# Kernel optimization log

Hardware: AMD Instinct MI355X
Metric: run time of the kernel (lower is better)

The kernel has to match this reference:

```python
import jax, jax.numpy as jnp
import numpy as np
from jax import lax

C = 128
HEADS = 8
WS = 8
HIDDEN = C * 4


def _ln2d(x, w, b, eps=1e-6):
    # channel-first LayerNorm over dim 1 of [B,C,H,W]
    u = x.mean(axis=1, keepdims=True)
    s = ((x - u) ** 2).mean(axis=1, keepdims=True)
    xh = (x - u) / jnp.sqrt(s + eps)
    return w[None, :, None, None] * xh + b[None, :, None, None]


def _partition(x, ws):
    # [B,C,H,W] -> [B*nW, ws*ws, C]
    B, C_, H, W = x.shape
    x = x.transpose(0, 2, 3, 1)  # BHWC
    x = x.reshape(B, H // ws, ws, W // ws, ws, C_)
    x = x.transpose(0, 1, 3, 2, 4, 5)
    return x.reshape(-1, ws * ws, C_)


def _reverse(x, ws, H, W, B):
    # [B*nW, ws*ws, C] -> [B,C,H,W]
    C_ = x.shape[-1]
    x = x.reshape(B, H // ws, W // ws, ws, ws, C_)
    x = x.transpose(0, 1, 3, 2, 4, 5).reshape(B, H, W, C_)
    return x.transpose(0, 3, 1, 2)


def setup_inputs() -> dict:
    key = jax.random.key(0)
    ks = jax.random.split(key, 16)
    B, H, W = 4, 256, 256
    inp = {
        "x": jax.random.normal(ks[0], (B, C, H, W), jnp.float32),
        "l0": jax.random.uniform(ks[1], (B, 1, H, W), jnp.float32),
        "norm1_w": jnp.ones((C,), jnp.float32),
        "norm1_b": jnp.zeros((C,), jnp.float32),
        "norm2_w": jnp.ones((C,), jnp.float32),
        "norm2_b": jnp.zeros((C,), jnp.float32),
        "qkv_w": jax.random.normal(ks[2], (3 * C, C), jnp.float32) * (1.0 / np.sqrt(C)),
        "gate_w": jax.random.normal(ks[3], (C,), jnp.float32),
        "gate_b": jnp.zeros((C,), jnp.float32),
        "proj_w": jax.random.normal(ks[4], (C, C), jnp.float32) * (1.0 / np.sqrt(C)),
        "proj_b": jnp.zeros((C,), jnp.float32),
        "ffn_w1": jax.random.normal(ks[5], (HIDDEN, C), jnp.float32) * (1.0 / np.sqrt(C)),
        "ffn_b1": jnp.zeros((HIDDEN,), jnp.float32),
        "ffn_dw": jax.random.normal(ks[6], (HIDDEN, 1, 3, 3), jnp.float32) * (1.0 / 3.0),
        "ffn_dwb": jnp.zeros((HIDDEN,), jnp.float32),
        "ffn_w2": jax.random.normal(ks[7], (C, HIDDEN), jnp.float32) * (1.0 / np.sqrt(HIDDEN)),
        "ffn_b2": jnp.zeros((C,), jnp.float32),
    }
    return inp


def reference(x, l0, norm1_w, norm1_b, norm2_w, norm2_b, qkv_w, gate_w, gate_b,
              proj_w, proj_b, ffn_w1, ffn_b1, ffn_dw, ffn_dwb, ffn_w2, ffn_b2):
    B, C_, H, W = x.shape
    ws = WS
    # H,W chosen divisible by ws -> no padding branch
    head_dim = C_ // HEADS
    scale = head_dim ** -0.5

    shortcut = x
    xn = _ln2d(x, norm1_w, norm1_b)
    qkv = jnp.einsum("oc,bchw->bohw", qkv_w, xn)
    q, k, v = jnp.split(qkv, 3, axis=1)

    # illumination gate (l0 already at [H,W]; bilinear resize to same size is identity)
    gate = jax.nn.sigmoid(l0 * gate_w[None, :, None, None] + gate_b[None, :, None, None])
    q = q * gate

    q = _partition(q, ws)  # [Bw, ws*ws, C]
    k = _partition(k, ws)
    v = _partition(v, ws)
    Bw, N, _ = q.shape
    q = q.reshape(Bw, N, HEADS, head_dim)
    k = k.reshape(Bw, N, HEADS, head_dim)
    v = v.reshape(Bw, N, HEADS, head_dim)

    attn = jnp.einsum("bqhd,bkhd->bhqk", q, k) * scale
    attn = jax.nn.softmax(attn, axis=-1)
    out = jnp.einsum("bhqk,bkhd->bqhd", attn, v).reshape(Bw, N, C_)
    out = _reverse(out, ws, H, W, B)

    out = jnp.einsum("oc,bchw->bohw", proj_w, out) + proj_b[None, :, None, None]
    out = out + shortcut

    # FFN: 1x1 -> GELU -> depthwise 3x3 -> GELU -> 1x1
    h = _ln2d(out, norm2_w, norm2_b)
    h = jnp.einsum("oc,bchw->bohw", ffn_w1, h) + ffn_b1[None, :, None, None]
    h = jax.nn.gelu(h, approximate=False)
    h = lax.conv_general_dilated(h, ffn_dw, window_strides=(1, 1), padding="SAME",
                                 dimension_numbers=("NCHW", "OIHW", "NCHW"),
                                 feature_group_count=HIDDEN)
    h = h + ffn_dwb[None, :, None, None]
    h = jax.nn.gelu(h, approximate=False)
    h = jnp.einsum("oc,bchw->bohw", ffn_w2, h) + ffn_b2[None, :, None, None]
    return out + h
```

## Files before the change

### kernel.cpp

```cpp
#include <hip/hip_runtime.h>
#include <hip/hip_bf16.h>

#define HW   65536
#define CHW  (128*65536)
#define QKV_OZ  33554432u
#define QKV_H   1048576u
#define QKV_WIN 1024u

typedef __attribute__((ext_vector_type(8))) short bf16x8;
typedef __attribute__((ext_vector_type(4))) float f32x4;

__device__ __forceinline__ float geluf(float v){
    float u = 0.7978845608028654f * v * (1.f + 0.044715f*v*v);
    float e = __expf(2.f*u);
    float th = 1.f - 2.f/(e+1.f);
    return 0.5f*v*(1.f+th);
}

__device__ __forceinline__ float sigmoidf_(float z){
    return 1.f / (1.f + __expf(-z));
}

__device__ __forceinline__ float bf2f(short s){
    return __uint_as_float(((unsigned)(unsigned short)s) << 16);
}

__global__ __launch_bounds__(256) void k_cvt(
    const float* __restrict__ src, __hip_bfloat16* __restrict__ dst, int n)
{
    int i = blockIdx.x*256 + threadIdx.x;
    if (i < n) dst[i] = __float2bfloat16(src[i]);
}

__global__ __launch_bounds__(256,2) void k_ln_qkv_mfma(
    const float* __restrict__ x, const float* __restrict__ l0,
    const float* __restrict__ n1w, const float* __restrict__ n1b,
    const __hip_bfloat16* __restrict__ qkvw, const float* __restrict__ gate_w,
    const float* __restrict__ gate_b, __hip_bfloat16* __restrict__ qkvb)
{
    __shared__ short sxb[128*130];
    __shared__ float sp1[256], sp2[256];
    const int t = threadIdx.x;
    const int lane = t & 63, w = t >> 6;
    const int l15 = lane & 15, q4 = (lane >> 4)*4, ko = (lane >> 4)*8;
    const int mhalf = w & 1, phalf = w >> 1;
    const int pbase = blockIdx.x * 128;
    const int b = pbase >> 16;
    const int hw0 = pbase & 65535;
    const int x0 = hw0 & 255;
    const int y  = hw0 >> 8;
    const int wy = y >> 3, ty = y & 7;
    const int pxs = t & 127, chalf = t >> 7;
    const float* xb = x + (size_t)b*CHW + (size_t)chalf*64*HW + hw0 + pxs;
    unsigned* srow = (unsigned*)sxb + pxs*65 + chalf*32;

    float s1 = 0.f, s2 = 0.f;
    #pragma unroll 8
    for (int j = 0; j < 32; ++j) {
        float v0 = xb[(size_t)(2*j)*HW];
        float v1 = xb[(size_t)(2*j+1)*HW];
        s1 += v0 + v1; s2 += v0*v0 + v1*v1;
        __hip_bfloat162 pk = __float22bfloat162_rn(make_float2(v0, v1));
        srow[j] = *(unsigned*)&pk;
    }
    sp1[pxs*2 + chalf] = s1;
    sp2[pxs*2 + chalf] = s2;
    __syncthreads();
    const float s1t = sp1[pxs*2] + sp1[pxs*2 + 1];
    const float s2t = sp2[pxs*2] + sp2[pxs*2 + 1];
    const float mean = s1t * 0.0078125f;
    const float rstd = rsqrtf(s2t*0.0078125f - mean*mean + 1e-6f);
    #pragma unroll 8
    for (int j = 0; j < 32; ++j) {
        unsigned u = srow[j];
        float v0 = __uint_as_float(u << 16);
        float v1 = __uint_as_float(u & 0xffff0000u);
        const int c = chalf*64 + 2*j;
        v0 = (v0 - mean)*rstd*n1w[c]   + n1b[c];
        v1 = (v1 - mean)*rstd*n1w[c+1] + n1b[c+1];
        __hip_bfloat162 pk = __float22bfloat162_rn(make_float2(v0, v1));
        srow[j] = *(unsigned*)&pk;
    }
    __syncthreads();

    float lv[4];
    #pragma unroll
    for (int nt = 0; nt < 4; ++nt)
        lv[nt] = l0[(size_t)b*HW + hw0 + phalf*64 + nt*16 + l15];

    unsigned toff[4];
    #pragma unroll
    for (int nt = 0; nt < 4; ++nt) {
        const int xg = x0 + phalf*64 + nt*16 + l15;
        toff[nt] = (unsigned)((wy*32 + (xg >> 3))*1024 + (ty*8 + (xg & 7))*16);
    }

    const short* wq = (const short*)qkvw;
    for (int oz = 0; oz < 3; ++oz) {
        f32x4 acc[4][4];
        #pragma unroll
        for (int mt = 0; mt < 4; ++mt)
            #pragma unroll
            for (int nt = 0; nt < 4; ++nt)
                acc[mt][nt] = (f32x4){0.f,0.f,0.f,0.f};
        #pragma unroll
        for (int kc = 0; kc < 4; ++kc) {
            bf16x8 bfrag[4];
            #pragma unroll
            for (int nt = 0; nt < 4; ++nt) {
                const int px = phalf*64 + nt*16 + l15;
                bfrag[nt] = *(const bf16x8*)(sxb + px*130 + kc*32 + ko);
            }
            #pragma unroll
            for (int mt = 0; mt < 4; ++mt) {
                const int m = oz*128 + mhalf*64 + mt*16 + l15;
                bf16x8 af = *(const bf16x8*)(wq + m*128 + kc*32 + ko);
                #pragma unroll
                for (int nt = 0; nt < 4; ++nt)
                    acc[mt][nt] = __builtin_amdgcn_mfma_f32_16x16x32_bf16(af, bfrag[nt], acc[mt][nt], 0, 0, 0);
            }
        }
        __hip_bfloat16* ob = qkvb + (size_t)oz*QKV_OZ + (size_t)b*8*QKV_H;
        #pragma unroll
        for (int mt = 0; mt < 4; ++mt) {
            const int h = mhalf*4 + mt;
            #pragma unroll
            for (int nt = 0; nt < 4; ++nt) {
                float v0 = acc[mt][nt][0], v1 = acc[mt][nt][1];
                float v2 = acc[mt][nt][2], v3 = acc[mt][nt][3];
                if (oz == 0) {
                    const int o = h*16 + q4;
                    v0 *= sigmoidf_(lv[nt]*gate_w[o]   + gate_b[o]);
                    v1 *= sigmoidf_(lv[nt]*gate_w[o+1] + gate_b[o+1]);
                    v2 *= sigmoidf_(lv[nt]*gate_w[o+2] + gate_b[o+2]);
                    v3 *= sigmoidf_(lv[nt]*gate_w[o+3] + gate_b[o+3]);
                }
                __hip_bfloat162 p0 = __float22bfloat162_rn(make_float2(v0, v1));
                __hip_bfloat162 p1 = __float22bfloat162_rn(make_float2(v2, v3));
                uint2 st;
                st.x = *(unsigned*)&p0;
                st.y = *(unsigned*)&p1;
                *(uint2*)(ob + (size_t)h*QKV_H + toff[nt] + q4) = st;
            }
        }
    }
}

__global__ __launch_bounds__(64) void k_attn(
    const __hip_bfloat16* __restrict__ qkv, float* __restrict__ attn_out)
{
    __shared__ float sk[64*17];
    __shared__ float sv[64*17];
    const int t = threadIdx.x;
    const int win = blockIdx.x;
    const int head = blockIdx.y;
    const int b = win >> 10;
    const int wi = win & 1023;
    const size_t wb = ((size_t)(b*8 + head))*QKV_H + (size_t)wi*QKV_WIN + t*16;
    const __hip_bfloat16* qp = qkv + wb;
    const __hip_bfloat16* kp = qp + QKV_OZ;
    const __hip_bfloat16* vp = qp + 2u*QKV_OZ;
    bf16x8 q0 = *(const bf16x8*)(qp);
    bf16x8 q1 = *(const bf16x8*)(qp + 8);
    bf16x8 k0 = *(const bf16x8*)(kp);
    bf16x8 k1 = *(const bf16x8*)(kp + 8);
    bf16x8 v0 = *(const bf16x8*)(vp);
    bf16x8 v1 = *(const bf16x8*)(vp + 8);
    float qr[16];
    #pragma unroll
    for (int j = 0; j < 8; ++j) {
        qr[j]   = bf2f(q0[j]);
        qr[8+j] = bf2f(q1[j]);
        sk[t*17 + j]     = bf2f(k0[j]);
        sk[t*17 + 8 + j] = bf2f(k1[j]);
        sv[t*17 + j]     = bf2f(v0[j]);
        sv[t*17 + 8 + j] = bf2f(v1[j]);
    }
    __syncthreads();
    float sc[64];
    float m = -1e30f;
    #pragma unroll
    for (int kt = 0; kt < 64; ++kt) {
        float dot = 0.f;
        #pragma unroll
        for (int d = 0; d < 16; ++d) dot = fmaf(qr[d], sk[kt*17+d], dot);
        dot *= 0.25f;
        sc[kt] = dot;
        m = fmaxf(m, dot);
    }
    float ssum = 0.f;
    #pragma unroll
    for (int kt = 0; kt < 64; ++kt) { float e = __expf(sc[kt]-m); sc[kt] = e; ssum += e; }
    const float rs = 1.f / ssum;
    float o[16];
    #pragma unroll
    for (int d = 0; d < 16; ++d) o[d] = 0.f;
    #pragma unroll
    for (int kt = 0; kt < 64; ++kt) {
        const float p = sc[kt];
        #pragma unroll
        for (int d = 0; d < 16; ++d) o[d] = fmaf(p, sv[kt*17+d], o[d]);
    }
    const int wy = wi >> 5, wx = wi & 31;
    const int ty = t >> 3, tx = t & 7;
    const size_t hw = (size_t)(wy*8 + ty)*256 + wx*8 + tx;
    float* ob = attn_out + (size_t)b*CHW + (size_t)head*16*HW + hw;
    #pragma unroll
    for (int d = 0; d < 16; ++d) ob[(size_t)d*HW] = o[d]*rs;
}

__global__ __launch_bounds__(256,2) void k_proj_mfma(
    const float* __restrict__ x, const __hip_bfloat16* __restrict__ projw,
    const float* __restrict__ proj_b, float* __restrict__ out)
{
    __shared__ short sxb[128*130];
    const int t = threadIdx.x;
    const int lane = t & 63, w = t >> 6;
    const int l15 = lane & 15, q4 = (lane >> 4)*4, ko = (lane >> 4)*8;
    const int mhalf = w & 1, phalf = w >> 1;
    const int pbase = blockIdx.x * 128;
    const int b = pbase >> 16;
    const int hw0 = pbase & 65535;
    const int pxs = t & 127, chalf = t >> 7;
    const float* ab = out + (size_t)b*CHW + (size_t)chalf*64*HW + hw0 + pxs;
    unsigned* srow = (unsigned*)sxb + pxs*65 + chalf*32;
    #pragma unroll 8
    for (int j = 0; j < 32; ++j) {
        float v0 = ab[(size_t)(2*j)*HW];
        float v1 = ab[(size_t)(2*j+1)*HW];
        __hip_bfloat162 pk = __float22bfloat162_rn(make_float2(v0, v1));
        srow[j] = *(unsigned*)&pk;
    }
    __syncthreads();
    f32x4 acc[4][4];
    #pragma unroll
    for (int mt = 0; mt < 4; ++mt)
        #pragma unroll
        for (int nt = 0; nt < 4; ++nt)
            acc[mt][nt] = (f32x4){0.f,0.f,0.f,0.f};
    const short* wp = (const short*)projw;
    #pragma unroll
    for (int kc = 0; kc < 4; ++kc) {
        bf16x8 bfrag[4];
        #pragma unroll
        for (int nt = 0; nt < 4; ++nt) {
            const int px = phalf*64 + nt*16 + l15;
            bfrag[nt] = *(const bf16x8*)(sxb + px*130 + kc*32 + ko);
        }
        #pragma unroll
        for (int mt = 0; mt < 4; ++mt) {
            const int m = mhalf*64 + mt*16 + l15;
            bf16x8 af = *(const bf16x8*)(wp + m*128 + kc*32 + ko);
            #pragma unroll
            for (int nt = 0; nt < 4; ++nt)
                acc[mt][nt] = __builtin_amdgcn_mfma_f32_16x16x32_bf16(af, bfrag[nt], acc[mt][nt], 0, 0, 0);
        }
    }
    const float* xb = x + (size_t)b*CHW + hw0;
    float* ob = out + (size_t)b*CHW + hw0;
    #pragma unroll
    for (int mt = 0; mt < 4; ++mt)
        #pragma unroll
        for (int nt = 0; nt < 4; ++nt) {
            const int px = phalf*64 + nt*16 + l15;
            #pragma unroll
            for (int r = 0; r < 4; ++r) {
                const int o = mhalf*64 + mt*16 + q4 + r;
                ob[(size_t)o*HW + px] = acc[mt][nt][r] + proj_b[o] + xb[(size_t)o*HW + px];
            }
        }
}

__global__ __launch_bounds__(256,2) void k_ffn1_mfma(
    const float* __restrict__ outb, const float* __restrict__ n2w, const float* __restrict__ n2b,
    const __hip_bfloat16* __restrict__ w1, const float* __restrict__ b1,
    __hip_bfloat16* __restrict__ h1s)
{
    __shared__ short sxb[128*130];
    __shared__ float sp1[256], sp2[256];
    const int t = threadIdx.x;
    const int lane = t & 63, w = t >> 6;
    const int l15 = lane & 15, q4 = (lane >> 4)*4, ko = (lane >> 4)*8;
    const int mhalf = w & 1, phalf = w >> 1;
    const int hw0 = blockIdx.x * 128;
    const int pxs = t & 127, chalf = t >> 7;
    const float* xb = outb + (size_t)chalf*64*HW + hw0 + pxs;
    unsigned* srow = (unsigned*)sxb + pxs*65 + chalf*32;
    float s1 = 0.f, s2 = 0.f;
    #pragma unroll 8
    for (int j = 0; j < 32; ++j) {
        float v0 = xb[(size_t)(2*j)*HW];
        float v1 = xb[(size_t)(2*j+1)*HW];
        s1 += v0 + v1; s2 += v0*v0 + v1*v1;
        __hip_bfloat162 pk = __float22bfloat162_rn(make_float2(v0, v1));
        srow[j] = *(unsigned*)&pk;
    }
    sp1[pxs*2 + chalf] = s1;
    sp2[pxs*2 + chalf] = s2;
    __syncthreads();
    const float s1t = sp1[pxs*2] + sp1[pxs*2 + 1];
    const float s2t = sp2[pxs*2] + sp2[pxs*2 + 1];
    const float mean = s1t * 0.0078125f;
    const float rstd = rsqrtf(s2t*0.0078125f - mean*mean + 1e-6f);
    #pragma unroll 8
    for (int j = 0; j < 32; ++j) {
        unsigned u = srow[j];
        float v0 = __uint_as_float(u << 16);
        float v1 = __uint_as_float(u & 0xffff0000u);
        const int c = chalf*64 + 2*j;
        v0 = (v0 - mean)*rstd*n2w[c]   + n2b[c];
        v1 = (v1 - mean)*rstd*n2w[c+1] + n2b[c+1];
        __hip_bfloat162 pk = __float22bfloat162_rn(make_float2(v0, v1));
        srow[j] = *(unsigned*)&pk;
    }
    __syncthreads();
    const short* w1s = (const short*)w1;
    __hip_bfloat16* hb = h1s + hw0;
    for (int mc = 0; mc < 4; ++mc) {
        f32x4 acc[4][4];
        #pragma unroll
        for (int mt = 0; mt < 4; ++mt)
            #pragma unroll
            for (int nt = 0; nt < 4; ++nt)
                acc[mt][nt] = (f32x4){0.f,0.f,0.f,0.f};
        #pragma unroll
        for (int kc = 0; kc < 4; ++kc) {
            bf16x8 bfrag[4];
            #pragma unroll
            for (int nt = 0; nt < 4; ++nt) {
                const int px = phalf*64 + nt*16 + l15;
                bfrag[nt] = *(const bf16x8*)(sxb + px*130 + kc*32 + ko);
            }
            #pragma unroll
            for (int mt = 0; mt < 4; ++mt) {
                const int m = mc*128 + mhalf*64 + mt*16 + l15;
                bf16x8 af = *(const bf16x8*)(w1s + m*128 + kc*32 + ko);
                #pragma unroll
                for (int nt = 0; nt < 4; ++nt)
                    acc[mt][nt] = __builtin_amdgcn_mfma_f32_16x16x32_bf16(af, bfrag[nt], acc[mt][nt], 0, 0, 0);
            }
        }
        #pragma unroll
        for (int mt = 0; mt < 4; ++mt)
            #pragma unroll
            for (int nt = 0; nt < 4; ++nt) {
                const int px = phalf*64 + nt*16 + l15;
                #pragma unroll
                for (int r = 0; r < 4; ++r) {
                    const int o = mc*128 + mhalf*64 + mt*16 + q4 + r;
                    const float v = geluf(acc[mt][nt][r] + b1[o]);
                    hb[(size_t)o*HW + px] = __float2bfloat16(v);
                }
            }
    }
}

__global__ __launch_bounds__(256) void k_dwconv(
    const __hip_bfloat16* __restrict__ h1b,
    unsigned* __restrict__ h2u,
    const float* __restrict__ dwf, const float* __restrict__ dwb)
{
    __shared__ short sh[2*18*260];
    const int t = threadIdx.x;
    const int rb = blockIdx.x & 15;
    const int cp = blockIdx.x >> 4;
    const int row0 = rb * 16;
    #pragma unroll
    for (int ch = 0; ch < 2; ++ch) {
        const __hip_bfloat16* src = h1b + (size_t)(cp*2 + ch)*HW;
        #pragma unroll
        for (int i = 0; i < 9; ++i) {
            const int idx = t + i*256;
            const int r = idx >> 7;
            const int u = idx & 127;
            const int y = row0 - 1 + r;
            unsigned v = 0u;
            if ((unsigned)y < 256u) v = *(const unsigned*)(src + (size_t)y*256 + u*2);
            *(unsigned*)(&sh[ch*4680 + r*260 + 2 + u*2]) = v;
        }
    }
    if (t < 72) {
        const int ch = t / 36, q = t - ch*36;
        const int r = q >> 1;
        sh[ch*4680 + r*260 + ((q & 1) ? 258 : 1)] = 0;
    }
    __syncthreads();
    float wt[2][9], bs[2];
    #pragma unroll
    for (int ch = 0; ch < 2; ++ch) {
        const float* dwc = dwf + (size_t)(cp*2 + ch)*9;
        #pragma unroll
        for (int k = 0; k < 9; ++k) wt[ch][k] = dwc[k];
        bs[ch] = dwb[cp*2 + ch];
    }
    const int xp = (t & 127) * 2;
    const int rh = t >> 7;
    #pragma unroll
    for (int r = 0; r < 8; ++r) {
        const int orow = rh*8 + r;
        const int y = row0 + orow;
        float res[2][2];
        #pragma unroll
        for (int ch = 0; ch < 2; ++ch) {
            const short* base = sh + ch*4680 + orow*260 + xp + 1;
            float a[3][4];
            #pragma unroll
            for (int dy = 0; dy < 3; ++dy)
                #pragma unroll
                for (int k = 0; k < 4; ++k)
                    a[dy][k] = __uint_as_float((unsigned)(unsigned short)base[dy*260 + k] << 16);
            #pragma unroll
            for (int xj = 0; xj < 2; ++xj) {
                float s = bs[ch];
                #pragma unroll
                for (int dy = 0; dy < 3; ++dy)
                    #pragma unroll
                    for (int dx = 0; dx < 3; ++dx)
                        s = fmaf(a[dy][xj+dx], wt[ch][dy*3+dx], s);
                res[ch][xj] = geluf(s);
            }
        }
        __hip_bfloat162 pk0 = __float22bfloat162_rn(make_float2(res[0][0], res[1][0]));
        __hip_bfloat162 pk1 = __float22bfloat162_rn(make_float2(res[0][1], res[1][1]));
        uint2 st;
        st.x = *(unsigned*)&pk0;
        st.y = *(unsigned*)&pk1;
        *(uint2*)(h2u + (size_t)cp*HW + (size_t)y*256 + xp) = st;
    }
}

__global__ __launch_bounds__(256,2) void k_ffn2g(
    const unsigned* __restrict__ h2u, const __hip_bfloat16* __restrict__ w2b,
    const float* __restrict__ b2, float* __restrict__ outb)
{
    __shared__ short sxb[128*130];
    const int t = threadIdx.x;
    const int lane = t & 63, w = t >> 6;
    const int l15 = lane & 15, q4 = (lane >> 4)*4, ko = (lane >> 4)*8;
    const int mhalf = w & 1, phalf = w >> 1;
    const int pbase = blockIdx.x * 128;
    const int pxs = t & 127;
    const int chalf = t >> 7;
    f32x4 acc[4][4];
    #pragma unroll
    for (int mt = 0; mt < 4; ++mt)
        #pragma unroll
        for (int nt = 0; nt < 4; ++nt)
            acc[mt][nt] = (f32x4){0.f,0.f,0.f,0.f};
    const short* w2s = (const short*)w2b;
    for (int k4 = 0; k4 < 4; ++k4) {
        if (k4) __syncthreads();
        const unsigned* hsrc = h2u + (size_t)(k4*64 + chalf*32)*HW + pbase + pxs;
        unsigned* sdst = (unsigned*)sxb + pxs*65 + chalf*32;
        #pragma unroll
        for (int c = 0; c < 32; ++c)
            sdst[c] = hsrc[(size_t)c*HW];
        __syncthreads();
        #pragma unroll
        for (int kc = 0; kc < 4; ++kc) {
            bf16x8 bfrag[4];
            #pragma unroll
            for (int nt = 0; nt < 4; ++nt) {
                const int px = phalf*64 + nt*16 + l15;
                bfrag[nt] = *(const bf16x8*)(sxb + px*130 + kc*32 + ko);
            }
            #pragma unroll
            for (int mt = 0; mt < 4; ++mt) {
                const int m = mhalf*64 + mt*16 + l15;
                bf16x8 af = *(const bf16x8*)(w2s + (size_t)m*512 + k4*128 + kc*32 + ko);
                #pragma unroll
                for (int nt = 0; nt < 4; ++nt)
                    acc[mt][nt] = __builtin_amdgcn_mfma_f32_16x16x32_bf16(af, bfrag[nt], acc[mt][nt], 0, 0, 0);
            }
        }
    }
    #pragma unroll
    for (int mt = 0; mt < 4; ++mt)
        #pragma unroll
        for (int nt = 0; nt < 4; ++nt) {
            const int px = pbase + phalf*64 + nt*16 + l15;
            #pragma unroll
            for (int r = 0; r < 4; ++r) {
                const int o = mhalf*64 + mt*16 + q4 + r;
                outb[(size_t)o*HW + px] = acc[mt][nt][r] + b2[o] + outb[(size_t)o*HW + px];
            }
        }
}

extern "C" void kernel_launch(void* const* d_in, const int* in_sizes, int n_in,
                              void* d_out, int out_size, void* d_ws, size_t ws_size,
                              hipStream_t stream) {
    const float* x      = (const float*)d_in[0];
    const float* l0     = (const float*)d_in[1];
    const float* n1w    = (const float*)d_in[2];
    const float* n1b    = (const float*)d_in[3];
    const float* n2w    = (const float*)d_in[4];
    const float* n2b    = (const float*)d_in[5];
    const float* qkv_w  = (const float*)d_in[6];
    const float* gate_w = (const float*)d_in[7];
    const float* gate_b = (const float*)d_in[8];
    const float* proj_w = (const float*)d_in[9];
    const float* proj_b = (const float*)d_in[10];
    const float* ffn_w1 = (const float*)d_in[11];
    const float* ffn_b1 = (const float*)d_in[12];
    const float* ffn_dw = (const float*)d_in[13];
    const float* ffn_dwb= (const float*)d_in[14];
    const float* ffn_w2 = (const float*)d_in[15];
    const float* ffn_b2 = (const float*)d_in[16];

    float* out = (float*)d_out;
    __hip_bfloat16* qkvb = (__hip_bfloat16*)d_ws;
    unsigned* h2u        = (unsigned*)d_ws;
    __hip_bfloat16* h1s  = (__hip_bfloat16*)((char*)d_ws + 201326592);
    char* wbase = (char*)d_ws + 268435456;
    __hip_bfloat16* qkvw_b = (__hip_bfloat16*)(wbase);
    __hip_bfloat16* projw_b= (__hip_bfloat16*)(wbase + 98304);
    __hip_bfloat16* w1b    = (__hip_bfloat16*)(wbase + 131072);
    __hip_bfloat16* w2b    = (__hip_bfloat16*)(wbase + 262144);

    k_cvt<<<dim3(192), dim3(256), 0, stream>>>(qkv_w, qkvw_b, 49152);
    k_cvt<<<dim3(64),  dim3(256), 0, stream>>>(proj_w, projw_b, 16384);
    k_cvt<<<dim3(256), dim3(256), 0, stream>>>(ffn_w1, w1b, 65536);
    k_cvt<<<dim3(256), dim3(256), 0, stream>>>(ffn_w2, w2b, 65536);

    k_ln_qkv_mfma<<<dim3(2048), dim3(256), 0, stream>>>(x, l0, n1w, n1b, qkvw_b, gate_w, gate_b, qkvb);
    k_attn       <<<dim3(4096, 8), dim3(64), 0, stream>>>(qkvb, out);
    k_proj_mfma  <<<dim3(2048), dim3(256), 0, stream>>>(x, projw_b, proj_b, out);
    for (int b = 0; b < 4; ++b) {
        k_ffn1_mfma<<<dim3(512),  dim3(256), 0, stream>>>(out + (size_t)b*CHW, n2w, n2b, w1b, ffn_b1, h1s);
        k_dwconv   <<<dim3(4096), dim3(256), 0, stream>>>(h1s, h2u, ffn_dw, ffn_dwb);
        k_ffn2g    <<<dim3(512),  dim3(256), 0, stream>>>(h2u, w2b, ffn_b2, out + (size_t)b*CHW);
    }
}
```

Before: 1.230 ms.

## Rewrite window attention with bf16 MFMA for QK^T and PV

Replaces the scalar per-thread attention kernel (one 64-thread block per window-head) with an MFMA-based kernel where each wavefront handles one window-head and four wavefronts share a block. QK^T and PV run as 16x16x32 bf16 MFMAs, with the unused half of K zero-padded. Probabilities are split into hi and lo bf16 parts and both are accumulated, so precision stays close to fp32. The aim is to remove the heavy scalar FMA and LDS traffic, at the cost of extra LDS transposes, block-wide syncs and a doubled PV pass.

```diff
diff --git a/kernel.cpp b/kernel.cpp
--- a/kernel.cpp
+++ b/kernel.cpp
@@ -8,6 +8,7 @@
 #define QKV_WIN 1024u
 
 typedef __attribute__((ext_vector_type(8))) short bf16x8;
+typedef __attribute__((ext_vector_type(4))) short bf16x4;
 typedef __attribute__((ext_vector_type(4))) float f32x4;
 
 __device__ __forceinline__ float geluf(float v){
@@ -146,67 +147,142 @@
     }
 }
 
-__global__ __launch_bounds__(64) void k_attn(
+__global__ __launch_bounds__(256) void k_attn(
     const __hip_bfloat16* __restrict__ qkv, float* __restrict__ attn_out)
 {
-    __shared__ float sk[64*17];
-    __shared__ float sv[64*17];
+    __shared__ short vt[4][16*72];
+    __shared__ short pt[4][64*68];
     const int t = threadIdx.x;
-    const int win = blockIdx.x;
-    const int head = blockIdx.y;
-    const int b = win >> 10;
-    const int wi = win & 1023;
-    const size_t wb = ((size_t)(b*8 + head))*QKV_H + (size_t)wi*QKV_WIN + t*16;
-    const __hip_bfloat16* qp = qkv + wb;
+    const int l = t & 63, w = t >> 6;
+    const int c = l & 15, g = l >> 4;
+    const int id = blockIdx.x*4 + w;
+    const int b = id >> 13;
+    const int head = (id >> 10) & 7;
+    const int wi = id & 1023;
+    const __hip_bfloat16* qp = qkv + ((size_t)(b*8 + head))*QKV_H + (size_t)wi*QKV_WIN;
     const __hip_bfloat16* kp = qp + QKV_OZ;
     const __hip_bfloat16* vp = qp + 2u*QKV_OZ;
-    bf16x8 q0 = *(const bf16x8*)(qp);
-    bf16x8 q1 = *(const bf16x8*)(qp + 8);
-    bf16x8 k0 = *(const bf16x8*)(kp);
-    bf16x8 k1 = *(const bf16x8*)(kp + 8);
-    bf16x8 v0 = *(const bf16x8*)(vp);
-    bf16x8 v1 = *(const bf16x8*)(vp + 8);
-    float qr[16];
-    #pragma unroll
-    for (int j = 0; j < 8; ++j) {
-        qr[j]   = bf2f(q0[j]);
-        qr[8+j] = bf2f(q1[j]);
-        sk[t*17 + j]     = bf2f(k0[j]);
-        sk[t*17 + 8 + j] = bf2f(k1[j]);
-        sv[t*17 + j]     = bf2f(v0[j]);
-        sv[t*17 + 8 + j] = bf2f(v1[j]);
-    }
-    __syncthreads();
-    float sc[64];
-    float m = -1e30f;
-    #pragma unroll
-    for (int kt = 0; kt < 64; ++kt) {
-        float dot = 0.f;
-        #pragma unroll
-        for (int d = 0; d < 16; ++d) dot = fmaf(qr[d], sk[kt*17+d], dot);
-        dot *= 0.25f;
-        sc[kt] = dot;
-        m = fmaxf(m, dot);
-    }
-    float ssum = 0.f;
-    #pragma unroll
-    for (int kt = 0; kt < 64; ++kt) { float e = __expf(sc[kt]-m); sc[kt] = e; ssum += e; }
-    const float rs = 1.f / ssum;
-    float o[16];
-    #pragma unroll
-    for (int d = 0; d < 16; ++d) o[d] = 0.f;
-    #pragma unroll
-    for (int kt = 0; kt < 64; ++kt) {
-        const float p = sc[kt];
-        #pragma unroll
-        for (int d = 0; d < 16; ++d) o[d] = fmaf(p, sv[kt*17+d], o[d]);
-    }
+
+    bf16x8 v0 = *(const bf16x8*)(vp + l*16);
+    bf16x8 v1 = *(const bf16x8*)(vp + l*16 + 8);
+    short* vtw = &vt[w][0];
+    #pragma unroll
+    for (int d = 0; d < 8; ++d) vtw[d*72 + l] = v0[d];
+    #pragma unroll
+    for (int d = 0; d < 8; ++d) vtw[(8+d)*72 + l] = v1[d];
+
+    bf16x8 kf[4], qf[4];
+    #pragma unroll
+    for (int mj = 0; mj < 4; ++mj) {
+        if (g < 2) {
+            kf[mj] = *(const bf16x8*)(kp + (mj*16 + c)*16 + g*8);
+            qf[mj] = *(const bf16x8*)(qp + (mj*16 + c)*16 + g*8);
+        } else {
+            kf[mj] = (bf16x8){0,0,0,0,0,0,0,0};
+            qf[mj] = (bf16x8){0,0,0,0,0,0,0,0};
+        }
+    }
+    f32x4 st[4][4];
+    #pragma unroll
+    for (int mj = 0; mj < 4; ++mj)
+        #pragma unroll
+        for (int ni = 0; ni < 4; ++ni)
+            st[mj][ni] = (f32x4){0.f,0.f,0.f,0.f};
+    #pragma unroll
+    for (int mj = 0; mj < 4; ++mj)
+        #pragma unroll
+        for (int ni = 0; ni < 4; ++ni)
+            st[mj][ni] = __builtin_amdgcn_mfma_f32_16x16x32_bf16(kf[mj], qf[ni], st[mj][ni], 0, 0, 0);
+
+    float rs[4];
+    bf16x4 pa[4][4], pb[4][4];
+    #pragma unroll
+    for (int ni = 0; ni < 4; ++ni) {
+        float mx = -1e30f;
+        #pragma unroll
+        for (int mj = 0; mj < 4; ++mj)
+            #pragma unroll
+            for (int r = 0; r < 4; ++r)
+                mx = fmaxf(mx, st[mj][ni][r]);
+        mx = fmaxf(mx, __shfl_xor(mx, 16));
+        mx = fmaxf(mx, __shfl_xor(mx, 32));
+        mx *= 0.25f;
+        float sum = 0.f;
+        #pragma unroll
+        for (int mj = 0; mj < 4; ++mj) {
+            float p[4], lo[4];
+            #pragma unroll
+            for (int r = 0; r < 4; ++r) {
+                p[r] = __expf(st[mj][ni][r]*0.25f - mx);
+                sum += p[r];
+            }
+            __hip_bfloat162 h0 = __float22bfloat162_rn(make_float2(p[0], p[1]));
+            __hip_bfloat162 h1 = __float22bfloat162_rn(make_float2(p[2], p[3]));
+            union { unsigned u[2]; bf16x4 v; } hi;
+            hi.u[0] = *(unsigned*)&h0; hi.u[1] = *(unsigned*)&h1;
+            pa[mj][ni] = hi.v;
+            #pragma unroll
+            for (int r = 0; r < 4; ++r) lo[r] = p[r] - bf2f(hi.v[r]);
+            __hip_bfloat162 g0 = __float22bfloat162_rn(make_float2(lo[0], lo[1]));
+            __hip_bfloat162 g1 = __float22bfloat162_rn(make_float2(lo[2], lo[3]));
+            union { unsigned u[2]; bf16x4 v; } lw;
+            lw.u[0] = *(unsigned*)&g0; lw.u[1] = *(unsigned*)&g1;
+            pb[mj][ni] = lw.v;
+        }
+        sum += __shfl_xor(sum, 16);
+        sum += __shfl_xor(sum, 32);
+        rs[ni] = 1.f / sum;
+    }
+
+    short* ptw = &pt[w][0];
+    f32x4 oc[4];
+    #pragma unroll
+    for (int ni = 0; ni < 4; ++ni) oc[ni] = (f32x4){0.f,0.f,0.f,0.f};
+    bf16x8 vf[2];
+    #pragma unroll
+    for (int kb = 0; kb < 2; ++kb)
+        vf[kb] = *(const bf16x8*)(vtw + c*72 + kb*32 + g*8);
+
+    #pragma unroll
+    for (int mj = 0; mj < 4; ++mj)
+        #pragma unroll
+        for (int ni = 0; ni < 4; ++ni)
+            *(bf16x4*)(ptw + (ni*16 + c)*68 + mj*16 + g*4) = pa[mj][ni];
+    __syncthreads();
+    #pragma unroll
+    for (int kb = 0; kb < 2; ++kb)
+        #pragma unroll
+        for (int ni = 0; ni < 4; ++ni) {
+            bf16x8 pf = *(const bf16x8*)(ptw + (ni*16 + c)*68 + kb*32 + g*8);
+            oc[ni] = __builtin_amdgcn_mfma_f32_16x16x32_bf16(vf[kb], pf, oc[ni], 0, 0, 0);
+        }
+    __syncthreads();
+    #pragma unroll
+    for (int mj = 0; mj < 4; ++mj)
+        #pragma unroll
+        for (int ni = 0; ni < 4; ++ni)
+            *(bf16x4*)(ptw + (ni*16 + c)*68 + mj*16 + g*4) = pb[mj][ni];
+    __syncthreads();
+    #pragma unroll
+    for (int kb = 0; kb < 2; ++kb)
+        #pragma unroll
+        for (int ni = 0; ni < 4; ++ni) {
+            bf16x8 pf = *(const bf16x8*)(ptw + (ni*16 + c)*68 + kb*32 + g*8);
+            oc[ni] = __builtin_amdgcn_mfma_f32_16x16x32_bf16(vf[kb], pf, oc[ni], 0, 0, 0);
+        }
+
     const int wy = wi >> 5, wx = wi & 31;
-    const int ty = t >> 3, tx = t & 7;
-    const size_t hw = (size_t)(wy*8 + ty)*256 + wx*8 + tx;
-    float* ob = attn_out + (size_t)b*CHW + (size_t)head*16*HW + hw;
-    #pragma unroll
-    for (int d = 0; d < 16; ++d) ob[(size_t)d*HW] = o[d]*rs;
+    float* ob = attn_out + (size_t)b*CHW + (size_t)(head*16)*HW + (size_t)(wy*8)*256 + wx*8;
+    #pragma unroll
+    for (int ni = 0; ni < 4; ++ni) {
+        const int tok = ni*16 + c;
+        float* o2 = ob + (tok >> 3)*256 + (tok & 7);
+        #pragma unroll
+        for (int r = 0; r < 4; ++r) {
+            const int d = g*4 + r;
+            o2[(size_t)d*HW] = oc[ni][r] * rs[ni];
+        }
+    }
 }
 
 __global__ __launch_bounds__(256,2) void k_proj_mfma(
@@ -524,7 +600,7 @@
     k_cvt<<<dim3(256), dim3(256), 0, stream>>>(ffn_w2, w2b, 65536);
 
     k_ln_qkv_mfma<<<dim3(2048), dim3(256), 0, stream>>>(x, l0, n1w, n1b, qkvw_b, gate_w, gate_b, qkvb);
-    k_attn       <<<dim3(4096, 8), dim3(64), 0, stream>>>(qkvb, out);
+    k_attn       <<<dim3(8192), dim3(256), 0, stream>>>(qkvb, out);
     k_proj_mfma  <<<dim3(2048), dim3(256), 0, stream>>>(x, projw_b, proj_b, out);
     for (int b = 0; b < 4; ++b) {
         k_ffn1_mfma<<<dim3(512),  dim3(256), 0, stream>>>(out + (size_t)b*CHW, n2w, n2b, w1b, ffn_b1, h1s);
```

Result: faster. 1.143 ms (-7.1%).
